# Performance work log

Measured on AMD Instinct MI355X. Metric: run time of the kernel, lower is better.

The kernel has to match this reference:

```python
import jax, jax.numpy as jnp
import numpy as np
from jax import lax

EPS = 1e-5

# sign binarization with straight-through-estimator gradient (identity),
# matching the .data-swap trick in BinarizeConv2d/BinarizeLinear.
@jax.custom_vjp
def ste_sign(x):
    return jnp.sign(x)

def _ste_fwd(x):
    return jnp.sign(x), None

def _ste_bwd(_, g):
    return (g,)

ste_sign.defvjp(_ste_fwd, _ste_bwd)


def conv3x3(x, w):
    # weight is binarized inside the layer; padding=1, stride=1, no bias
    return lax.conv_general_dilated(
        x, ste_sign(w), window_strides=(1, 1), padding=((1, 1), (1, 1)),
        dimension_numbers=('NCHW', 'OIHW', 'NCHW'))


def mp2(x):
    return lax.reduce_window(x, -jnp.inf, lax.max, (1, 1, 2, 2), (1, 1, 2, 2), 'VALID')


def bn2d(x, gamma, beta):
    # training-mode BatchNorm2d: batch statistics over (N, H, W)
    mu = jnp.mean(x, axis=(0, 2, 3), keepdims=True)
    var = jnp.var(x, axis=(0, 2, 3), keepdims=True)
    xn = (x - mu) * lax.rsqrt(var + EPS)
    return xn * gamma[None, :, None, None] + beta[None, :, None, None]


def bn1d(x, gamma=None, beta=None):
    mu = jnp.mean(x, axis=0, keepdims=True)
    var = jnp.var(x, axis=0, keepdims=True)
    xn = (x - mu) * lax.rsqrt(var + EPS)
    if gamma is None:
        return xn
    return xn * gamma[None, :] + beta[None, :]


def hardtanh(x):
    return jnp.clip(x, -1.0, 1.0)


def setup_inputs() -> dict:
    key = jax.random.key(0)
    ks = jax.random.split(key, 16)
    def w(k, shape):
        return jax.random.normal(k, shape, jnp.float32) * 0.1
    d = {'x': jax.random.normal(ks[0], (512, 3, 32, 32), jnp.float32)}
    convs = [(64, 3), (64, 64), (128, 64), (128, 128), (256, 128), (256, 256)]
    for i, (co, ci) in enumerate(convs):
        d[f'w{i+1}'] = w(ks[1 + i], (co, ci, 3, 3))
        d[f'g{i+1}'] = jnp.ones((co,), jnp.float32)
        d[f'b{i+1}'] = jnp.zeros((co,), jnp.float32)
    d['wf1'] = w(ks[7], (512, 256 * 4 * 4))
    d['gf1'] = jnp.ones((512,), jnp.float32)
    d['bf1'] = jnp.zeros((512,), jnp.float32)
    d['wf2'] = w(ks[8], (512, 512))
    d['gf2'] = jnp.ones((512,), jnp.float32)
    d['bf2'] = jnp.zeros((512,), jnp.float32)
    d['wf3'] = w(ks[9], (10, 512))
    return d


def reference(x, w1, g1, b1, w2, g2, b2, w3, g3, b3, w4, g4, b4,
              w5, g5, b5, w6, g6, b6, wf1, gf1, bf1, wf2, gf2, bf2, wf3):
    # block 1: first conv sees raw 3-channel input (not binarized)
    h = hardtanh(bn2d(conv3x3(x, w1), g1, b1))
    h = hardtanh(bn2d(mp2(conv3x3(ste_sign(h), w2)), g2, b2))
    # block 2
    h = hardtanh(bn2d(conv3x3(ste_sign(h), w3), g3, b3))
    h = hardtanh(bn2d(mp2(conv3x3(ste_sign(h), w4)), g4, b4))
    # block 3
    h = hardtanh(bn2d(conv3x3(ste_sign(h), w5), g5, b5))
    h = hardtanh(bn2d(mp2(conv3x3(ste_sign(h), w6)), g6, b6))
    # classifier (all linear inputs binarized: feature dim != 784)
    h = h.reshape(-1, 256 * 4 * 4)
    h = hardtanh(bn1d(ste_sign(h) @ ste_sign(wf1).T, gf1, bf1))
    h = hardtanh(bn1d(ste_sign(h) @ ste_sign(wf2).T, gf2, bf2))
    h = bn1d(ste_sign(h) @ ste_sign(wf3).T)  # affine=False
    return jax.nn.log_softmax(h, axis=-1)
```

## Files before the change

### kernel.cpp

```cpp
#include <hip/hip_runtime.h>
#include <stdint.h>
#include <math.h>


typedef unsigned long long u64;

__device__ __forceinline__ void flag_and_wave(u64* flag, u64 nz) {
    nz &= __shfl_xor(nz, 1);
    nz &= __shfl_xor(nz, 2);
    nz &= __shfl_xor(nz, 4);
    nz &= __shfl_xor(nz, 8);
    nz &= __shfl_xor(nz, 16);
    nz &= __shfl_xor(nz, 32);
    if ((threadIdx.x & 63) == 0) atomicAnd(flag, nz);
}

__global__ void kflag_init(u64* __restrict__ f) {
    int i = threadIdx.x;
    if (i < 16) f[i] = ~0ull;
}

__global__ __launch_bounds__(256) void k1_conv_allv(const float* __restrict__ x,
                                                    const float* __restrict__ wt,
                                                    float* __restrict__ out) {
    int gid = blockIdx.x * 256 + threadIdx.x;
    int n = gid >> 8, hw0 = (gid & 255) * 4;
    int y = hw0 >> 5, x0 = hw0 & 31;
    const float* ip = x + (size_t)n * 3 * 1024;
    for (int c0 = 0; c0 < 64; c0 += 16) {
        float4 a[16];
#pragma unroll
        for (int c = 0; c < 16; ++c) a[c] = make_float4(0.f, 0.f, 0.f, 0.f);
        for (int ky = 0; ky < 3; ++ky) {
            int yy = y + ky - 1;
            bool rowok = (unsigned)yy < 32u;
            float win[3][6];
#pragma unroll
            for (int ci = 0; ci < 3; ++ci)
#pragma unroll
                for (int j = 0; j < 6; ++j) {
                    int cc = x0 - 1 + j;
                    bool ok = rowok && ((unsigned)cc < 32u);
                    win[ci][j] = ok ? ip[ci * 1024 + yy * 32 + cc] : 0.f;
                }
#pragma unroll
            for (int kx = 0; kx < 3; ++kx)
#pragma unroll
                for (int ci = 0; ci < 3; ++ci) {
                    const float* wrow = wt + (ci * 9 + ky * 3 + kx) * 64 + c0;
                    float s0 = win[ci][kx], s1 = win[ci][kx + 1];
                    float s2 = win[ci][kx + 2], s3 = win[ci][kx + 3];
#pragma unroll
                    for (int c = 0; c < 16; ++c) {
                        float wv = wrow[c];
                        a[c].x = fmaf(wv, s0, a[c].x);
                        a[c].y = fmaf(wv, s1, a[c].y);
                        a[c].z = fmaf(wv, s2, a[c].z);
                        a[c].w = fmaf(wv, s3, a[c].w);
                    }
                }
        }
#pragma unroll
        for (int c = 0; c < 16; ++c)
            *(float4*)(out + ((size_t)n * 64 + c0 + c) * 1024 + hw0) = a[c];
    }
}

__global__ void k1_statsA(const float* __restrict__ v, double* __restrict__ Sp,
                          double* __restrict__ S2p, int N) {
    int c = blockIdx.x;
    int slot = blockIdx.y * 64 + threadIdx.x;
    double s = 0.0, s2 = 0.0;
    int K = N * 4;
    const float* vp = v + (size_t)c * 1024 + slot;
    int k0 = 0;
    for (; k0 + 32 <= K; k0 += 32) {
        const float* p0 = vp + (size_t)(k0 >> 2) * 65536;
        float buf[32];
#pragma unroll
        for (int j = 0; j < 32; ++j)
            buf[j] = p0[(size_t)(j >> 2) * 65536 + (j & 3) * 256];
#pragma unroll
        for (int j = 0; j < 32; ++j) {
            double t = (double)buf[j];
            s += t; s2 += t * t;
        }
    }
    for (; k0 < K; ++k0) {
        int m = slot + k0 * 256;
        double t = (double)v[((size_t)(m >> 10) * 64 + c) * 1024 + (m & 1023)];
        s += t; s2 += t * t;
    }
    Sp[c * 256 + slot] = s; S2p[c * 256 + slot] = s2;
}

__global__ void k1_statsB(const double* __restrict__ Sp, const double* __restrict__ S2p,
                          float* __restrict__ muF, float* __restrict__ rF, int N) {
    int c = blockIdx.x;
    __shared__ double sh[256], sh2[256];
    sh[threadIdx.x]  = Sp[c * 256 + threadIdx.x];
    sh2[threadIdx.x] = S2p[c * 256 + threadIdx.x];
    __syncthreads();
    for (int o = 128; o > 0; o >>= 1) {
        if ((int)threadIdx.x < o) { sh[threadIdx.x] += sh[threadIdx.x + o]; sh2[threadIdx.x] += sh2[threadIdx.x + o]; }
        __syncthreads();
    }
    if (threadIdx.x == 0) {
        int M = N * 1024;
        double mean = sh[0] / M;
        double var  = sh2[0] / M - mean * mean;
        if (var < 0.0) var = 0.0;
        muF[c] = (float)mean;
        rF[c]  = 1.0f / sqrtf((float)var + 1e-5f);
    }
}

__global__ void k1_signpack(const float* __restrict__ v, const float* __restrict__ muF,
                            const float* __restrict__ rF, const float* __restrict__ g,
                            const float* __restrict__ b, u64* __restrict__ B,
                            u64* __restrict__ NZ, u64* __restrict__ aflag) {
    int gid = blockIdx.x * 64 + threadIdx.x;
    int n = gid >> 8, hw0 = (gid & 255) * 4;
    const float* vp = v + ((size_t)n * 64) * 1024 + hw0;
    u64 bb0 = 0, bb1 = 0, bb2 = 0, bb3 = 0;
    u64 nz0 = 0, nz1 = 0, nz2 = 0, nz3 = 0;
    for (int c0 = 0; c0 < 64; c0 += 16) {
        float4 buf[16];
#pragma unroll
        for (int j = 0; j < 16; ++j)
            buf[j] = *(const float4*)(vp + (size_t)(c0 + j) * 1024);
#pragma unroll
        for (int j = 0; j < 16; ++j) {
            int c = c0 + j;
            float mc = muF[c], rc = rF[c], gc = g[c], bc = b[c];
            float d0 = buf[j].x - mc; float t0 = (d0 * rc) * gc + bc;
            float d1 = buf[j].y - mc; float t1 = (d1 * rc) * gc + bc;
            float d2 = buf[j].z - mc; float t2 = (d2 * rc) * gc + bc;
            float d3 = buf[j].w - mc; float t3 = (d3 * rc) * gc + bc;
            bb0 |= (u64)(t0 > 0.f) << c;  nz0 |= (u64)(t0 != 0.f) << c;
            bb1 |= (u64)(t1 > 0.f) << c;  nz1 |= (u64)(t1 != 0.f) << c;
            bb2 |= (u64)(t2 > 0.f) << c;  nz2 |= (u64)(t2 != 0.f) << c;
            bb3 |= (u64)(t3 > 0.f) << c;  nz3 |= (u64)(t3 != 0.f) << c;
        }
    }
    size_t o = (size_t)n * 1024 + hw0;
    B[o]     = bb0; B[o + 1]  = bb1; B[o + 2]  = bb2; B[o + 3]  = bb3;
    NZ[o]    = nz0; NZ[o + 1] = nz1; NZ[o + 2] = nz2; NZ[o + 3] = nz3;
    flag_and_wave(aflag, nz0 & nz1 & nz2 & nz3);
}

__global__ void k1_conv(const float* __restrict__ x, const float* __restrict__ w1,
                        float* __restrict__ out, int grp) {
    int hw = blockIdx.x * 64 + threadIdx.x;
    int cg = blockIdx.y;
    int n  = blockIdx.z;
    int co = grp * 8 + cg;
    int y = hw >> 5, x0 = hw & 31;
    const float* ip0 = x + ((size_t)n * 3 + 0) * 1024;
    const float* ip1 = x + ((size_t)n * 3 + 1) * 1024;
    const float* ip2 = x + ((size_t)n * 3 + 2) * 1024;
    const float* wp  = w1 + (size_t)co * 27;
    float acc = 0.f;
    for (int ky = 0; ky < 3; ++ky) {
        int yy = y + ky - 1;
        if (yy < 0 || yy > 31) continue;
        for (int kx = 0; kx < 3; ++kx) {
            int xc = x0 + kx - 1;
            if (xc < 0 || xc > 31) continue;
            int sp = yy * 32 + xc;
            int wk = ky * 3 + kx;
            float w0 = wp[wk], w1v = wp[9 + wk], w2 = wp[18 + wk];
            acc += (w0  > 0.f) ? ip0[sp] : ((w0  < 0.f) ? -ip0[sp] : 0.f);
            acc += (w1v > 0.f) ? ip1[sp] : ((w1v < 0.f) ? -ip1[sp] : 0.f);
            acc += (w2  > 0.f) ? ip2[sp] : ((w2  < 0.f) ? -ip2[sp] : 0.f);
        }
    }
    out[((size_t)n * 8 + cg) * 1024 + hw] = acc;
}

__device__ __forceinline__ float ld1(const float* v, int cg, int e) {
    return v[((size_t)(e >> 10) * 8 + cg) * 1024 + (e & 1023)];
}

__global__ void k1_stats(const float* __restrict__ v, float* __restrict__ muF,
                         float* __restrict__ rF, int grp, int N) {
    int cg = blockIdx.x;
    __shared__ double sh[256], sh2[256];
    double s = 0.0, s2 = 0.0;
    int M = N * 1024;
    for (int m = threadIdx.x; m < M; m += 256) {
        double t = (double)ld1(v, cg, m);
        s += t; s2 += t * t;
    }
    sh[threadIdx.x] = s; sh2[threadIdx.x] = s2;
    __syncthreads();
    for (int o = 128; o > 0; o >>= 1) {
        if ((int)threadIdx.x < o) { sh[threadIdx.x] += sh[threadIdx.x + o]; sh2[threadIdx.x] += sh2[threadIdx.x + o]; }
        __syncthreads();
    }
    if (threadIdx.x == 0) {
        double mean = sh[0] / M;
        double var  = sh2[0] / M - mean * mean;
        if (var < 0.0) var = 0.0;
        muF[grp * 8 + cg] = (float)mean;
        rF[grp * 8 + cg]  = 1.0f / sqrtf((float)var + 1e-5f);
    }
}

__global__ void k1_sign(const float* __restrict__ v, const float* __restrict__ muF,
                        const float* __restrict__ rF, const float* __restrict__ g,
                        const float* __restrict__ b, int8_t* __restrict__ sgn, int grp) {
    int hw = blockIdx.x * 256 + threadIdx.x;
    if (hw >= 1024) return;
    int cg = blockIdx.y, n = blockIdx.z;
    int c = grp * 8 + cg;
    float d  = v[((size_t)n * 8 + cg) * 1024 + hw] - muF[c];
    float t  = (d * rF[c]) * g[c] + b[c];
    sgn[((size_t)n * 64 + c) * 1024 + hw] = (int8_t)((t > 0.f) - (t < 0.f));
}

__global__ void kpack_sgn8(const int8_t* __restrict__ s, u64* __restrict__ B,
                           u64* __restrict__ NZ, int C, int HW, u64* __restrict__ aflag) {
    int hw = blockIdx.x * 64 + threadIdx.x;
    int wd = blockIdx.y, n = blockIdx.z;
    int WRD = C >> 6;
    u64 b = 0, nz = ~0ull;
    if (hw < HW) {
        nz = 0;
        const int8_t* sp = s + ((size_t)n * C + wd * 64) * HW + hw;
        for (int j = 0; j < 64; ++j) {
            int v = sp[(size_t)j * HW];
            b  |= (u64)(v > 0) << j;
            nz |= (u64)(v != 0) << j;
        }
        size_t o = ((size_t)n * HW + hw) * WRD + wd;
        B[o] = b; NZ[o] = nz;
    }
    flag_and_wave(aflag, nz);
}

__device__ __forceinline__ void pack_wconv_body(const float* __restrict__ w,
                                                u64* __restrict__ WB, u64* __restrict__ WNZ,
                                                int Ci, int Co, u64* flag, int idx) {
    int WRD = Ci >> 6;
    u64 b = 0, nz = ~0ull;
    if (idx < Co * 9 * WRD) {
        nz = 0;
        int wd = idx % WRD, t = (idx / WRD) % 9, co = idx / (9 * WRD);
        const float* wp = w + ((size_t)co * Ci + wd * 64) * 9 + t;
        float buf[64];
#pragma unroll
        for (int j = 0; j < 64; ++j) buf[j] = wp[(size_t)j * 9];
#pragma unroll
        for (int j = 0; j < 64; ++j) {
            b  |= (u64)(buf[j] > 0.f) << j;
            nz |= (u64)(buf[j] != 0.f) << j;
        }
        WB[idx] = b; WNZ[idx] = nz;
    }
    flag_and_wave(flag, nz);
}

__device__ __forceinline__ void pack_wlinT_body(const float* __restrict__ w,
                                                u64* __restrict__ WBt, u64* __restrict__ WZt,
                                                int K, int O, u64* flag, int idx) {
    int WRD = K >> 6;
    u64 b = 0, nz = ~0ull;
    if (idx < O * WRD) {
        nz = 0;
        int wd = idx % WRD, o = idx / WRD;
        const float* wp = w + (size_t)o * K + wd * 64;
#pragma unroll 8
        for (int j = 0; j < 64; ++j) {
            float v = wp[j];
            b  |= (u64)(v > 0.f) << j;
            nz |= (u64)(v != 0.f) << j;
        }
        WBt[(size_t)wd * O + o] = b; WZt[(size_t)wd * O + o] = nz;
    }
    flag_and_wave(flag, nz);
}

__global__ void kpack_all(const float* __restrict__ w1, const float* __restrict__ w2,
                          const float* __restrict__ w3, const float* __restrict__ w4,
                          const float* __restrict__ w5, const float* __restrict__ w6,
                          const float* __restrict__ wf1, const float* __restrict__ wf2,
                          const float* __restrict__ wf3, float* __restrict__ wt,
                          u64* wb2B, u64* wb2Z, u64* wb3B, u64* wb3Z,
                          u64* wb4B, u64* wb4Z, u64* wb5B, u64* wb5Z,
                          u64* wb6B, u64* wb6Z, u64* wf1B, u64* wf1Z,
                          u64* wf2B, u64* wf2Z, u64* wf3B, u64* wf3Z,
                          u64* flags) {
    int b = blockIdx.x, t = threadIdx.x;
    if      (b <   3) pack_wconv_body(w2, wb2B, wb2Z,  64,  64, &flags[0], b * 256 + t);
    else if (b <   8) pack_wconv_body(w3, wb3B, wb3Z,  64, 128, &flags[1], (b - 3) * 256 + t);
    else if (b <  17) pack_wconv_body(w4, wb4B, wb4Z, 128, 128, &flags[2], (b - 8) * 256 + t);
    else if (b <  35) pack_wconv_body(w5, wb5B, wb5Z, 128, 256, &flags[3], (b - 17) * 256 + t);
    else if (b <  71) pack_wconv_body(w6, wb6B, wb6Z, 256, 256, &flags[4], (b - 35) * 256 + t);
    else if (b < 199) pack_wlinT_body(wf1, wf1B, wf1Z, 4096, 512, &flags[5], (b - 71) * 256 + t);
    else if (b < 215) pack_wlinT_body(wf2, wf2B, wf2Z,  512, 512, &flags[6], (b - 199) * 256 + t);
    else if (b < 216) pack_wlinT_body(wf3, wf3B, wf3Z,  512,  10, &flags[7], (b - 215) * 256 + t);
    else {
        int i = (b - 216) * 256 + t;
        if (i < 64 * 27) {
            int co = i / 27, k = i % 27;
            float v = w1[i];
            wt[k * 64 + co] = (v > 0.f) ? 1.f : ((v < 0.f) ? -1.f : 0.f);
        }
    }
}

template <int WRD, int CB>
__device__ __forceinline__ void conv_slow(const u64* __restrict__ ib, const u64* __restrict__ iz,
                                          const u64* __restrict__ wbp, const u64* __restrict__ wzp,
                                          int H, int Wi, int y, int x, int* acc) {
#pragma unroll
    for (int c = 0; c < CB; ++c) acc[c] = 0;
    for (int ky = 0; ky < 3; ++ky) {
        int yy = y + ky - 1;
        if ((unsigned)yy >= (unsigned)H) continue;
        for (int kx = 0; kx < 3; ++kx) {
            int xc = x + kx - 1;
            if ((unsigned)xc >= (unsigned)Wi) continue;
            int p = yy * Wi + xc, t = ky * 3 + kx;
            u64 xb[WRD], xz[WRD];
#pragma unroll
            for (int w = 0; w < WRD; ++w) {
                xb[w] = ib[(size_t)p * WRD + w];
                xz[w] = iz[(size_t)p * WRD + w];
            }
#pragma unroll
            for (int c = 0; c < CB; ++c) {
#pragma unroll
                for (int w = 0; w < WRD; ++w) {
                    u64 e = xz[w] & wzp[(c * 9 + t) * WRD + w];
                    acc[c] += __popcll(e) - 2 * __popcll((xb[w] ^ wbp[(c * 9 + t) * WRD + w]) & e);
                }
            }
        }
    }
}

template <int WRD, int CB>
__device__ __forceinline__ void conv_fast(const u64* __restrict__ ib,
                                          const u64* __restrict__ wbp,
                                          int H, int Wi, int y, int x, int* acc) {
    int a2[CB];
#pragma unroll
    for (int c = 0; c < CB; ++c) a2[c] = 0;
    int T = 0;
    for (int ky = 0; ky < 3; ++ky) {
        int yy = y + ky - 1;
        if ((unsigned)yy >= (unsigned)H) continue;
        for (int kx = 0; kx < 3; ++kx) {
            int xc = x + kx - 1;
            if ((unsigned)xc >= (unsigned)Wi) continue;
            int p = yy * Wi + xc, t = ky * 3 + kx;
            ++T;
            u64 xb[WRD];
#pragma unroll
            for (int w = 0; w < WRD; ++w) xb[w] = ib[(size_t)p * WRD + w];
#pragma unroll
            for (int c = 0; c < CB; ++c)
#pragma unroll
                for (int w = 0; w < WRD; ++w)
                    a2[c] += __popcll(xb[w] ^ wbp[(c * 9 + t) * WRD + w]);
        }
    }
#pragma unroll
    for (int c = 0; c < CB; ++c) acc[c] = 64 * WRD * T - 2 * a2[c];
}

template <int WRD, int CB>
__global__ void kbconv2(const u64* __restrict__ B, const u64* __restrict__ NZ,
                        const u64* __restrict__ WB, const u64* __restrict__ WNZ,
                        int16_t* __restrict__ out, int Co, int H, int Wi,
                        const u64* __restrict__ wflag, const u64* __restrict__ aflag) {
    int hw = blockIdx.x * 64 + threadIdx.x;
    if (hw >= H * Wi) return;
    int co0 = blockIdx.y * CB, n = blockIdx.z;
    int y = hw / Wi, x = hw % Wi;
    const u64* ib = B  + (size_t)n * H * Wi * WRD;
    const u64* iz = NZ + (size_t)n * H * Wi * WRD;
    const u64* wbp = WB  + (size_t)co0 * 9 * WRD;
    const u64* wzp = WNZ + (size_t)co0 * 9 * WRD;
    bool fast = ((*wflag) & (*aflag)) == ~0ull;
    int acc[CB];
    if (fast) conv_fast<WRD, CB>(ib, wbp, H, Wi, y, x, acc);
    else      conv_slow<WRD, CB>(ib, iz, wbp, wzp, H, Wi, y, x, acc);
#pragma unroll
    for (int c = 0; c < CB; ++c)
        out[((size_t)n * Co + co0 + c) * H * Wi + hw] = (int16_t)acc[c];
}

template <int WRD, int CB>
__global__ void kbconv_pool2(const u64* __restrict__ B, const u64* __restrict__ NZ,
                             const u64* __restrict__ WB, const u64* __restrict__ WNZ,
                             int16_t* __restrict__ out, int Co, int H, int Wi,
                             const u64* __restrict__ wflag, const u64* __restrict__ aflag) {
    int Ho = H >> 1, Wo = Wi >> 1;
    int hw = blockIdx.x * 64 + threadIdx.x;
    if (hw >= Ho * Wo) return;
    int co0 = blockIdx.y * CB, n = blockIdx.z;
    int yo = hw / Wo, xo = hw % Wo;
    const u64* ib = B  + (size_t)n * H * Wi * WRD;
    const u64* iz = NZ + (size_t)n * H * Wi * WRD;
    const u64* wbp = WB  + (size_t)co0 * 9 * WRD;
    const u64* wzp = WNZ + (size_t)co0 * 9 * WRD;
    bool fast = ((*wflag) & (*aflag)) == ~0ull;
    int best[CB];
#pragma unroll
    for (int c = 0; c < CB; ++c) best[c] = -(1 << 30);
    if (fast) {
        for (int dy = 0; dy < 2; ++dy)
            for (int dx = 0; dx < 2; ++dx) {
                int acc[CB];
                conv_fast<WRD, CB>(ib, wbp, H, Wi, 2 * yo + dy, 2 * xo + dx, acc);
#pragma unroll
                for (int c = 0; c < CB; ++c) best[c] = acc[c] > best[c] ? acc[c] : best[c];
            }
    } else {
        for (int dy = 0; dy < 2; ++dy)
            for (int dx = 0; dx < 2; ++dx) {
                int acc[CB];
                conv_slow<WRD, CB>(ib, iz, wbp, wzp, H, Wi, 2 * yo + dy, 2 * xo + dx, acc);
#pragma unroll
                for (int c = 0; c < CB; ++c) best[c] = acc[c] > best[c] ? acc[c] : best[c];
            }
    }
#pragma unroll
    for (int c = 0; c < CB; ++c)
        out[((size_t)n * Co + co0 + c) * Ho * Wo + hw] = (int16_t)best[c];
}

template <int WRD, int CB>
__global__ void kbconv_pool2s(const u64* __restrict__ B, const u64* __restrict__ NZ,
                              const u64* __restrict__ WB, const u64* __restrict__ WNZ,
                              int16_t* __restrict__ out, int Co, int H, int Wi,
                              const u64* __restrict__ wflag, const u64* __restrict__ aflag) {
    int Ho = H >> 1, Wo = Wi >> 1;
    int t0 = threadIdx.x;
    int pix = t0 & 15, pos = t0 >> 4;
    int co0 = blockIdx.y * CB, n = blockIdx.z;
    int yo = pix / Wo, xo = pix % Wo;
    int y = 2 * yo + (pos >> 1), x = 2 * xo + (pos & 1);
    const u64* ib = B  + (size_t)n * H * Wi * WRD;
    const u64* iz = NZ + (size_t)n * H * Wi * WRD;
    const u64* wbp = WB  + (size_t)co0 * 9 * WRD;
    const u64* wzp = WNZ + (size_t)co0 * 9 * WRD;
    bool fast = ((*wflag) & (*aflag)) == ~0ull;
    int acc[CB];
    if (fast) conv_fast<WRD, CB>(ib, wbp, H, Wi, y, x, acc);
    else      conv_slow<WRD, CB>(ib, iz, wbp, wzp, H, Wi, y, x, acc);
#pragma unroll
    for (int c = 0; c < CB; ++c) {
        int v = acc[c];
        int v1 = __shfl_xor(v, 16); v = v1 > v ? v1 : v;
        int v2 = __shfl_xor(v, 32); v = v2 > v ? v2 : v;
        acc[c] = v;
    }
    if (pos == 0) {
#pragma unroll
        for (int c = 0; c < CB; ++c)
            out[((size_t)n * Co + co0 + c) * Ho * Wo + pix] = (int16_t)acc[c];
    }
}

__global__ void kaccum16(const int16_t* __restrict__ v, long long* __restrict__ Sp,
                         long long* __restrict__ S2p, int C, int HW, int M) {
    int c = blockIdx.x;
    long long s = 0, s2 = 0;
    int M8 = M >> 3;
    for (int g = blockIdx.y * 256 + threadIdx.x; g < M8; g += gridDim.y * 256) {
        int m0 = g * 8;
        const int16_t* p = v + ((size_t)(m0 / HW) * C + c) * HW + (m0 % HW);
        short4 a = *(const short4*)p;
        short4 b = *(const short4*)(p + 4);
        int v0 = a.x, v1 = a.y, v2 = a.z, v3 = a.w;
        int v4 = b.x, v5 = b.y, v6 = b.z, v7 = b.w;
        s  += v0 + v1 + v2 + v3 + v4 + v5 + v6 + v7;
        s2 += (long long)v0 * v0 + (long long)v1 * v1 + (long long)v2 * v2 + (long long)v3 * v3
            + (long long)v4 * v4 + (long long)v5 * v5 + (long long)v6 * v6 + (long long)v7 * v7;
    }
    __shared__ long long sh[256], sh2[256];
    sh[threadIdx.x] = s; sh2[threadIdx.x] = s2;
    __syncthreads();
    for (int o = 128; o > 0; o >>= 1) {
        if ((int)threadIdx.x < o) { sh[threadIdx.x] += sh[threadIdx.x + o]; sh2[threadIdx.x] += sh2[threadIdx.x + o]; }
        __syncthreads();
    }
    if (threadIdx.x == 0) {
        Sp[c * gridDim.y + blockIdx.y]  = sh[0];
        S2p[c * gridDim.y + blockIdx.y] = sh2[0];
    }
}

__global__ void kfinal2(const long long* __restrict__ Sp, const long long* __restrict__ S2p,
                        int NB, const float* __restrict__ g, const float* __restrict__ b,
                        double* __restrict__ mu, double* __restrict__ Ad,
                        double* __restrict__ Bd, int C, int M) {
    int c = blockIdx.x * 64 + threadIdx.x;
    if (c >= C) return;
    long long s = 0, s2 = 0;
    for (int i = 0; i < NB; ++i) { s += Sp[c * NB + i]; s2 += S2p[c * NB + i]; }
    double mean = (double)s / M;
    double var  = (double)s2 / M - mean * mean;
    if (var < 0.0) var = 0.0;
    mu[c] = mean;
    Ad[c] = (g ? (double)g[c] : 1.0) / sqrt(var + 1e-5);
    Bd[c] = b ? (double)b[c] : 0.0;
}

__global__ void ksp_conv(const int16_t* __restrict__ v, const double* __restrict__ mu,
                         const double* __restrict__ Ad, const double* __restrict__ Bd,
                         u64* __restrict__ B, u64* __restrict__ NZ, int C, int HW, int N,
                         u64* __restrict__ aflag) {
    int tid = blockIdx.x * 64 + threadIdx.x;
    int WRD = C >> 6;
    int HW4 = HW >> 2;
    int total = N * WRD * HW4;
    u64 nzall = ~0ull;
    if (tid < total) {
        int hw4 = tid % HW4;
        int wd  = (tid / HW4) % WRD;
        int n   = tid / (HW4 * WRD);
        const int16_t* vp = v + ((size_t)n * C + wd * 64) * HW + hw4 * 4;
        u64 b0 = 0, b1 = 0, b2 = 0, b3 = 0;
        u64 n0 = 0, n1 = 0, n2 = 0, n3 = 0;
        for (int j0 = 0; j0 < 64; j0 += 16) {
            short4 buf[16];
#pragma unroll
            for (int j = 0; j < 16; ++j)
                buf[j] = *(const short4*)(vp + (size_t)(j0 + j) * HW);
#pragma unroll
            for (int j = 0; j < 16; ++j) {
                int c = wd * 64 + j0 + j;
                double Mu = mu[c], A = Ad[c], Bb = Bd[c];
                double t0 = ((double)buf[j].x - Mu) * A + Bb;
                double t1 = ((double)buf[j].y - Mu) * A + Bb;
                double t2 = ((double)buf[j].z - Mu) * A + Bb;
                double t3 = ((double)buf[j].w - Mu) * A + Bb;
                int sh = j0 + j;
                b0 |= (u64)(t0 > 0.0) << sh;  n0 |= (u64)(t0 != 0.0) << sh;
                b1 |= (u64)(t1 > 0.0) << sh;  n1 |= (u64)(t1 != 0.0) << sh;
                b2 |= (u64)(t2 > 0.0) << sh;  n2 |= (u64)(t2 != 0.0) << sh;
                b3 |= (u64)(t3 > 0.0) << sh;  n3 |= (u64)(t3 != 0.0) << sh;
            }
        }
        size_t o = ((size_t)n * HW + hw4 * 4) * WRD + wd;
        B[o] = b0;  B[o + WRD] = b1;  B[o + 2 * WRD] = b2;  B[o + 3 * WRD] = b3;
        NZ[o] = n0; NZ[o + WRD] = n1; NZ[o + 2 * WRD] = n2; NZ[o + 3 * WRD] = n3;
        nzall = n0 & n1 & n2 & n3;
    }
    flag_and_wave(aflag, nzall);
}

__global__ void ksp_flat(const int16_t* __restrict__ v, const double* __restrict__ mu,
                         const double* __restrict__ Ad, const double* __restrict__ Bd,
                         u64* __restrict__ B, u64* __restrict__ NZ, u64* __restrict__ aflag) {
    int wd = threadIdx.x;
    int n  = blockIdx.x;
    const int16_t* vp = v + (size_t)n * 4096 + wd * 64;
    int16_t buf[64];
#pragma unroll
    for (int j = 0; j < 64; ++j) buf[j] = vp[j];
    u64 b = 0, nz = 0;
#pragma unroll
    for (int j = 0; j < 64; ++j) {
        int k = wd * 64 + j;
        int c = k >> 4;
        double t = ((double)buf[j] - mu[c]) * Ad[c] + Bd[c];
        b  |= (u64)(t > 0.0) << j;
        nz |= (u64)(t != 0.0) << j;
    }
    B[(size_t)n * 64 + wd] = b; NZ[(size_t)n * 64 + wd] = nz;
    flag_and_wave(aflag, nz);
}

__global__ void ksp_fc(const int* __restrict__ v, const double* __restrict__ mu,
                       const double* __restrict__ Ad, const double* __restrict__ Bd,
                       u64* __restrict__ B, u64* __restrict__ NZ, int C, int WRD, int N,
                       u64* __restrict__ aflag) {
    int tid = blockIdx.x * 64 + threadIdx.x;
    u64 nz = ~0ull;
    if (tid < N * WRD) {
        int n = tid / WRD, wd = tid % WRD;
        const int* vp = v + (size_t)n * C + wd * 64;
        int buf[64];
#pragma unroll
        for (int j = 0; j < 64; ++j) buf[j] = vp[j];
        u64 b = 0; nz = 0;
#pragma unroll
        for (int j = 0; j < 64; ++j) {
            int c = wd * 64 + j;
            double t = ((double)buf[j] - mu[c]) * Ad[c] + Bd[c];
            b  |= (u64)(t > 0.0) << j;
            nz |= (u64)(t != 0.0) << j;
        }
        B[(size_t)n * WRD + wd] = b; NZ[(size_t)n * WRD + wd] = nz;
    }
    flag_and_wave(aflag, nz);
}

__global__ void kbfc(const u64* __restrict__ aB, const u64* __restrict__ aNZ,
                     const u64* __restrict__ wBt, const u64* __restrict__ wZt,
                     int* __restrict__ out, int WRD, int O,
                     const u64* __restrict__ wflag, const u64* __restrict__ aflag) {
    int o = blockIdx.x * 64 + threadIdx.x;
    if (o >= O) return;
    int n = blockIdx.y;
    const u64* ab = aB  + (size_t)n * WRD;
    const u64* az = aNZ + (size_t)n * WRD;
    bool fast = ((*wflag) & (*aflag)) == ~0ull;
    int acc;
    if (fast) {
        int a2 = 0;
        for (int w = 0; w < WRD; w += 8) {
            u64 aw[8], ww[8];
#pragma unroll
            for (int j = 0; j < 8; ++j) {
                aw[j] = ab[w + j];
                ww[j] = wBt[(size_t)(w + j) * O + o];
            }
#pragma unroll
            for (int j = 0; j < 8; ++j) a2 += __popcll(aw[j] ^ ww[j]);
        }
        acc = 64 * WRD - 2 * a2;
    } else {
        acc = 0;
        for (int w = 0; w < WRD; ++w) {
            u64 wb = wBt[(size_t)w * O + o];
            u64 wz = wZt[(size_t)w * O + o];
            u64 e = az[w] & wz;
            acc += __popcll(e) - 2 * __popcll((ab[w] ^ wb) & e);
        }
    }
    out[(size_t)n * O + o] = acc;
}

__global__ void k3_stats(const int* __restrict__ v, int N, int C,
                         const float* __restrict__ g, const float* __restrict__ b,
                         double* __restrict__ mu, double* __restrict__ Ad,
                         double* __restrict__ Bd) {
    int c = blockIdx.x;
    __shared__ double sh[256], sh2[256];
    double s = 0.0, s2 = 0.0;
    for (int n = threadIdx.x; n < N; n += 256) {
        double t = (double)v[(size_t)n * C + c];
        s += t; s2 += t * t;
    }
    sh[threadIdx.x] = s; sh2[threadIdx.x] = s2;
    __syncthreads();
    for (int o = 128; o > 0; o >>= 1) {
        if ((int)threadIdx.x < o) { sh[threadIdx.x] += sh[threadIdx.x + o]; sh2[threadIdx.x] += sh2[threadIdx.x + o]; }
        __syncthreads();
    }
    if (threadIdx.x == 0) {
        double mean = sh[0] / N;
        double var  = sh2[0] / N - mean * mean;
        if (var < 0.0) var = 0.0;
        mu[c] = mean;
        Ad[c] = (g ? (double)g[c] : 1.0) / sqrt(var + 1e-5);
        Bd[c] = b ? (double)b[c] : 0.0;
    }
}

__global__ void k4_out(const int* __restrict__ v, const double* __restrict__ mu,
                       const double* __restrict__ Ad, float* __restrict__ out, int N) {
    int n = blockIdx.x * 256 + threadIdx.x;
    if (n >= N) return;
    double z[10];
    double mx = -1e300;
    for (int o = 0; o < 10; ++o) {
        z[o] = ((double)v[n * 10 + o] - mu[o]) * Ad[o];
        if (z[o] > mx) mx = z[o];
    }
    double s = 0.0;
    for (int o = 0; o < 10; ++o) s += exp(z[o] - mx);
    double l = mx + log(s);
    for (int o = 0; o < 10; ++o) out[n * 10 + o] = (float)(z[o] - l);
}

extern "C" void kernel_launch(void* const* d_in, const int* in_sizes, int n_in,
                              void* d_out, int out_size, void* d_ws, size_t ws_size,
                              hipStream_t stream) {
    const int N = in_sizes[0] / (3 * 32 * 32);

    const float* x   = (const float*)d_in[0];
    const float* w1  = (const float*)d_in[1];
    const float* g1  = (const float*)d_in[2];
    const float* b1  = (const float*)d_in[3];
    const float* w2  = (const float*)d_in[4];
    const float* g2  = (const float*)d_in[5];
    const float* b2  = (const float*)d_in[6];
    const float* w3  = (const float*)d_in[7];
    const float* g3  = (const float*)d_in[8];
    const float* b3  = (const float*)d_in[9];
    const float* w4  = (const float*)d_in[10];
    const float* g4  = (const float*)d_in[11];
    const float* b4  = (const float*)d_in[12];
    const float* w5  = (const float*)d_in[13];
    const float* g5  = (const float*)d_in[14];
    const float* b5  = (const float*)d_in[15];
    const float* w6  = (const float*)d_in[16];
    const float* g6  = (const float*)d_in[17];
    const float* b6  = (const float*)d_in[18];
    const float* wf1 = (const float*)d_in[19];
    const float* gf1 = (const float*)d_in[20];
    const float* bf1 = (const float*)d_in[21];
    const float* wf2 = (const float*)d_in[22];
    const float* gf2 = (const float*)d_in[23];
    const float* bf2 = (const float*)d_in[24];
    const float* wf3 = (const float*)d_in[25];

    char* ws = (char*)d_ws;
    size_t off = 0;
    auto alloc = [&](size_t bytes) -> char* {
        char* p = ws + off;
        off = (off + bytes + 511) & ~(size_t)511;
        return p;
    };

    int16_t* t2  = (int16_t*)alloc((size_t)N * 64 * 256 * 2);
    u64* p2B = (u64*)alloc((size_t)N * 256 * 8);
    u64* p2Z = (u64*)alloc((size_t)N * 256 * 8);
    int16_t* t3  = (int16_t*)alloc((size_t)N * 128 * 256 * 2);
    u64* p3B = (u64*)alloc((size_t)N * 256 * 2 * 8);
    u64* p3Z = (u64*)alloc((size_t)N * 256 * 2 * 8);
    int16_t* t4  = (int16_t*)alloc((size_t)N * 128 * 64 * 2);
    u64* p4B = (u64*)alloc((size_t)N * 64 * 2 * 8);
    u64* p4Z = (u64*)alloc((size_t)N * 64 * 2 * 8);
    int16_t* t5  = (int16_t*)alloc((size_t)N * 256 * 64 * 2);
    u64* p5B = (u64*)alloc((size_t)N * 64 * 4 * 8);
    u64* p5Z = (u64*)alloc((size_t)N * 64 * 4 * 8);
    int16_t* t6  = (int16_t*)alloc((size_t)N * 256 * 16 * 2);
    u64* p6B = (u64*)alloc((size_t)N * 64 * 8);
    u64* p6Z = (u64*)alloc((size_t)N * 64 * 8);
    int* fc1 = (int*)alloc((size_t)N * 512 * 4);
    int* fc2 = (int*)alloc((size_t)N * 512 * 4);
    int* fc3 = (int*)alloc((size_t)N * 10 * 4);
    u64* pF1B = (u64*)alloc((size_t)N * 8 * 8);
    u64* pF1Z = (u64*)alloc((size_t)N * 8 * 8);
    u64* pF2B = (u64*)alloc((size_t)N * 8 * 8);
    u64* pF2Z = (u64*)alloc((size_t)N * 8 * 8);
    size_t down_end = off;

    size_t head_big = (size_t)N * 64 * 1024 * 4;
    bool big = ws_size >= head_big + ((size_t)20 << 20);
    float*  c1buf = (float*)ws;
    float*  c1buf8 = (float*)ws;
    int8_t* sgnA  = (int8_t*)(ws + (size_t)N * 8 * 1024 * 4);

    off = big ? (head_big > down_end ? head_big : down_end) : down_end;
    off = (off + 511) & ~(size_t)511;
    u64* p1B = (u64*)alloc((size_t)N * 1024 * 8);
    u64* p1Z = (u64*)alloc((size_t)N * 1024 * 8);
    u64* wb2B = (u64*)alloc(64  * 9 * 1 * 8);  u64* wb2Z = (u64*)alloc(64  * 9 * 1 * 8);
    u64* wb3B = (u64*)alloc(128 * 9 * 1 * 8);  u64* wb3Z = (u64*)alloc(128 * 9 * 1 * 8);
    u64* wb4B = (u64*)alloc(128 * 9 * 2 * 8);  u64* wb4Z = (u64*)alloc(128 * 9 * 2 * 8);
    u64* wb5B = (u64*)alloc(256 * 9 * 2 * 8);  u64* wb5Z = (u64*)alloc(256 * 9 * 2 * 8);
    u64* wb6B = (u64*)alloc(256 * 9 * 4 * 8);  u64* wb6Z = (u64*)alloc(256 * 9 * 4 * 8);
    u64* wf1B = (u64*)alloc(512 * 64 * 8);     u64* wf1Z = (u64*)alloc(512 * 64 * 8);
    u64* wf2B = (u64*)alloc(512 * 8 * 8);      u64* wf2Z = (u64*)alloc(512 * 8 * 8);
    u64* wf3B = (u64*)alloc(10 * 8 * 8);       u64* wf3Z = (u64*)alloc(10 * 8 * 8);
    float* wt = (float*)alloc(27 * 64 * 4);
    double* Sp  = (double*)alloc(64 * 256 * 8);
    double* S2p = (double*)alloc(64 * 256 * 8);
    long long* SpI  = (long long*)alloc(256 * 32 * 8);
    long long* S2pI = (long long*)alloc(256 * 32 * 8);
    u64* flags = (u64*)alloc(16 * 8);
    double* mu = (double*)alloc(512 * 8);
    double* Ad = (double*)alloc(512 * 8);
    double* Bd = (double*)alloc(512 * 8);
    float*  muF = (float*)alloc(64 * 4);
    float*  rF  = (float*)alloc(64 * 4);

    auto cdiv = [](int a, int b) { return (a + b - 1) / b; };

    kflag_init<<<1, 64, 0, stream>>>(flags);
    kpack_all<<<223, 256, 0, stream>>>(w1, w2, w3, w4, w5, w6, wf1, wf2, wf3, wt,
                                       wb2B, wb2Z, wb3B, wb3Z, wb4B, wb4Z,
                                       wb5B, wb5Z, wb6B, wb6Z, wf1B, wf1Z,
                                       wf2B, wf2Z, wf3B, wf3Z, flags);

    if (big) {
        k1_conv_allv<<<(N * 256) / 256, 256, 0, stream>>>(x, wt, c1buf);
        k1_statsA<<<dim3(64, 4), 64, 0, stream>>>(c1buf, Sp, S2p, N);
        k1_statsB<<<64, 256, 0, stream>>>(Sp, S2p, muF, rF, N);
        k1_signpack<<<(N * 256) / 64, 64, 0, stream>>>(c1buf, muF, rF, g1, b1, p1B, p1Z, &flags[8]);
    } else {
        for (int grp = 0; grp < 8; ++grp) {
            k1_conv<<<dim3(16, 8, N), 64, 0, stream>>>(x, w1, c1buf8, grp);
            k1_stats<<<8, 256, 0, stream>>>(c1buf8, muF, rF, grp, N);
            k1_sign<<<dim3(4, 8, N), 256, 0, stream>>>(c1buf8, muF, rF, g1, b1, sgnA, grp);
        }
        kpack_sgn8<<<dim3(16, 1, N), 64, 0, stream>>>(sgnA, p1B, p1Z, 64, 1024, &flags[8]);
    }

    kbconv_pool2<1, 8><<<dim3(4, 8, N), 64, 0, stream>>>(p1B, p1Z, wb2B, wb2Z, t2, 64, 32, 32, &flags[0], &flags[8]);
    kaccum16<<<dim3(64, 32), 256, 0, stream>>>(t2, SpI, S2pI, 64, 256, N * 256);
    kfinal2<<<1, 64, 0, stream>>>(SpI, S2pI, 32, g2, b2, mu, Ad, Bd, 64, N * 256);
    ksp_conv<<<cdiv(N * 1 * 64, 64), 64, 0, stream>>>(t2, mu, Ad, Bd, p2B, p2Z, 64, 256, N, &flags[9]);

    kbconv2<1, 8><<<dim3(4, 16, N), 64, 0, stream>>>(p2B, p2Z, wb3B, wb3Z, t3, 128, 16, 16, &flags[1], &flags[9]);
    kaccum16<<<dim3(128, 16), 256, 0, stream>>>(t3, SpI, S2pI, 128, 256, N * 256);
    kfinal2<<<2, 64, 0, stream>>>(SpI, S2pI, 16, g3, b3, mu, Ad, Bd, 128, N * 256);
    ksp_conv<<<cdiv(N * 2 * 64, 64), 64, 0, stream>>>(t3, mu, Ad, Bd, p3B, p3Z, 128, 256, N, &flags[10]);

    kbconv_pool2<2, 8><<<dim3(1, 16, N), 64, 0, stream>>>(p3B, p3Z, wb4B, wb4Z, t4, 128, 16, 16, &flags[2], &flags[10]);
    kaccum16<<<dim3(128, 16), 256, 0, stream>>>(t4, SpI, S2pI, 128, 64, N * 64);
    kfinal2<<<2, 64, 0, stream>>>(SpI, S2pI, 16, g4, b4, mu, Ad, Bd, 128, N * 64);
    ksp_conv<<<cdiv(N * 2 * 16, 64), 64, 0, stream>>>(t4, mu, Ad, Bd, p4B, p4Z, 128, 64, N, &flags[11]);

    kbconv2<2, 8><<<dim3(1, 32, N), 64, 0, stream>>>(p4B, p4Z, wb5B, wb5Z, t5, 256, 8, 8, &flags[3], &flags[11]);
    kaccum16<<<dim3(256, 8), 256, 0, stream>>>(t5, SpI, S2pI, 256, 64, N * 64);
    kfinal2<<<4, 64, 0, stream>>>(SpI, S2pI, 8, g5, b5, mu, Ad, Bd, 256, N * 64);
    ksp_conv<<<cdiv(N * 4 * 16, 64), 64, 0, stream>>>(t5, mu, Ad, Bd, p5B, p5Z, 256, 64, N, &flags[12]);

    kbconv_pool2s<4, 8><<<dim3(1, 32, N), 64, 0, stream>>>(p5B, p5Z, wb6B, wb6Z, t6, 256, 8, 8, &flags[4], &flags[12]);
    kaccum16<<<dim3(256, 2), 256, 0, stream>>>(t6, SpI, S2pI, 256, 16, N * 16);
    kfinal2<<<4, 64, 0, stream>>>(SpI, S2pI, 2, g6, b6, mu, Ad, Bd, 256, N * 16);
    ksp_flat<<<N, 64, 0, stream>>>(t6, mu, Ad, Bd, p6B, p6Z, &flags[13]);

    kbfc<<<dim3(8, N), 64, 0, stream>>>(p6B, p6Z, wf1B, wf1Z, fc1, 64, 512, &flags[5], &flags[13]);
    k3_stats<<<512, 256, 0, stream>>>(fc1, N, 512, gf1, bf1, mu, Ad, Bd);
    ksp_fc<<<cdiv(N * 8, 64), 64, 0, stream>>>(fc1, mu, Ad, Bd, pF1B, pF1Z, 512, 8, N, &flags[14]);

    kbfc<<<dim3(8, N), 64, 0, stream>>>(pF1B, pF1Z, wf2B, wf2Z, fc2, 8, 512, &flags[6], &flags[14]);
    k3_stats<<<512, 256, 0, stream>>>(fc2, N, 512, gf2, bf2, mu, Ad, Bd);
    ksp_fc<<<cdiv(N * 8, 64), 64, 0, stream>>>(fc2, mu, Ad, Bd, pF2B, pF2Z, 512, 8, N, &flags[15]);

    kbfc<<<dim3(1, N), 64, 0, stream>>>(pF2B, pF2Z, wf3B, wf3Z, fc3, 8, 10, &flags[7], &flags[15]);
    k3_stats<<<10, 256, 0, stream>>>(fc3, N, 10, nullptr, nullptr, mu, Ad, Bd);
    k4_out<<<cdiv(N, 256), 256, 0, stream>>>(fc3, mu, Ad, (float*)d_out, N);
}
```

Before: 652.7 us.

## Reuse loaded activation windows across neighbouring outputs in binary convs

Adds a conv kernel where each thread computes two horizontally adjacent output pixels from one 3x4 register window. Each weight word is loaded once and applied to both pixels, and the result is stored as a packed 32-bit write. The pool2 fast path now loads a 4x4 input window once and reuses it for all four pooled positions instead of calling conv_fast four times. This cuts redundant global loads of activations and weights, at the cost of more registers and fewer threads for layer 3.

```diff
diff --git a/kernel.cpp b/kernel.cpp
--- a/kernel.cpp
+++ b/kernel.cpp
@@ -394,6 +394,76 @@
 }
 
 template <int WRD, int CB>
+__global__ void kbconv2p(const u64* __restrict__ B, const u64* __restrict__ NZ,
+                         const u64* __restrict__ WB, const u64* __restrict__ WNZ,
+                         int16_t* __restrict__ out, int Co, int H, int Wi,
+                         const u64* __restrict__ wflag, const u64* __restrict__ aflag) {
+    int W2 = Wi >> 1;
+    int hp = blockIdx.x * 64 + threadIdx.x;
+    if (hp >= H * W2) return;
+    int co0 = blockIdx.y * CB, n = blockIdx.z;
+    int y = hp / W2, x0 = (hp % W2) * 2;
+    const u64* ib = B  + (size_t)n * H * Wi * WRD;
+    const u64* iz = NZ + (size_t)n * H * Wi * WRD;
+    const u64* wbp = WB  + (size_t)co0 * 9 * WRD;
+    const u64* wzp = WNZ + (size_t)co0 * 9 * WRD;
+    bool fast = ((*wflag) & (*aflag)) == ~0ull;
+    int acc0[CB], acc1[CB];
+    if (fast) {
+        u64 xr[3][4][WRD]; bool vr[3][4];
+#pragma unroll
+        for (int dy = 0; dy < 3; ++dy) {
+            int yy = y - 1 + dy;
+            bool rok = (unsigned)yy < (unsigned)H;
+#pragma unroll
+            for (int dx = 0; dx < 4; ++dx) {
+                int xc = x0 - 1 + dx;
+                bool ok = rok && ((unsigned)xc < (unsigned)Wi);
+                vr[dy][dx] = ok;
+#pragma unroll
+                for (int w = 0; w < WRD; ++w)
+                    xr[dy][dx][w] = ok ? ib[(size_t)(yy * Wi + xc) * WRD + w] : 0ull;
+            }
+        }
+        int a20[CB], a21[CB];
+#pragma unroll
+        for (int c = 0; c < CB; ++c) { a20[c] = 0; a21[c] = 0; }
+        int T0 = 0, T1 = 0;
+#pragma unroll
+        for (int ky = 0; ky < 3; ++ky)
+#pragma unroll
+            for (int kx = 0; kx < 3; ++kx) {
+                int t = ky * 3 + kx;
+                bool v0 = vr[ky][kx], v1 = vr[ky][kx + 1];
+                if (v0) ++T0;
+                if (v1) ++T1;
+#pragma unroll
+                for (int c = 0; c < CB; ++c)
+#pragma unroll
+                    for (int w = 0; w < WRD; ++w) {
+                        u64 wv = wbp[(c * 9 + t) * WRD + w];
+                        if (v0) a20[c] += __popcll(xr[ky][kx][w] ^ wv);
+                        if (v1) a21[c] += __popcll(xr[ky][kx + 1][w] ^ wv);
+                    }
+            }
+#pragma unroll
+        for (int c = 0; c < CB; ++c) {
+            acc0[c] = 64 * WRD * T0 - 2 * a20[c];
+            acc1[c] = 64 * WRD * T1 - 2 * a21[c];
+        }
+    } else {
+        conv_slow<WRD, CB>(ib, iz, wbp, wzp, H, Wi, y, x0, acc0);
+        conv_slow<WRD, CB>(ib, iz, wbp, wzp, H, Wi, y, x0 + 1, acc1);
+    }
+#pragma unroll
+    for (int c = 0; c < CB; ++c) {
+        unsigned pack = (unsigned)(uint16_t)(int16_t)acc0[c]
+                      | ((unsigned)(uint16_t)(int16_t)acc1[c] << 16);
+        *(unsigned*)&out[((size_t)n * Co + co0 + c) * H * Wi + y * Wi + x0] = pack;
+    }
+}
+
+template <int WRD, int CB>
 __global__ void kbconv_pool2(const u64* __restrict__ B, const u64* __restrict__ NZ,
                              const u64* __restrict__ WB, const u64* __restrict__ WNZ,
                              int16_t* __restrict__ out, int Co, int H, int Wi,
@@ -412,12 +482,47 @@
 #pragma unroll
     for (int c = 0; c < CB; ++c) best[c] = -(1 << 30);
     if (fast) {
-        for (int dy = 0; dy < 2; ++dy)
-            for (int dx = 0; dx < 2; ++dx) {
-                int acc[CB];
-                conv_fast<WRD, CB>(ib, wbp, H, Wi, 2 * yo + dy, 2 * xo + dx, acc);
-#pragma unroll
-                for (int c = 0; c < CB; ++c) best[c] = acc[c] > best[c] ? acc[c] : best[c];
+        u64 xr[4][4][WRD]; bool vr[4][4];
+#pragma unroll
+        for (int dy = 0; dy < 4; ++dy) {
+            int yy = 2 * yo - 1 + dy;
+            bool rok = (unsigned)yy < (unsigned)H;
+#pragma unroll
+            for (int dx = 0; dx < 4; ++dx) {
+                int xc = 2 * xo - 1 + dx;
+                bool ok = rok && ((unsigned)xc < (unsigned)Wi);
+                vr[dy][dx] = ok;
+#pragma unroll
+                for (int w = 0; w < WRD; ++w)
+                    xr[dy][dx][w] = ok ? ib[(size_t)(yy * Wi + xc) * WRD + w] : 0ull;
+            }
+        }
+#pragma unroll
+        for (int dy2 = 0; dy2 < 2; ++dy2)
+#pragma unroll
+            for (int dx2 = 0; dx2 < 2; ++dx2) {
+                int a2[CB];
+#pragma unroll
+                for (int c = 0; c < CB; ++c) a2[c] = 0;
+                int T = 0;
+#pragma unroll
+                for (int ky = 0; ky < 3; ++ky)
+#pragma unroll
+                    for (int kx = 0; kx < 3; ++kx) {
+                        if (!vr[dy2 + ky][dx2 + kx]) continue;
+                        ++T;
+                        int t = ky * 3 + kx;
+#pragma unroll
+                        for (int c = 0; c < CB; ++c)
+#pragma unroll
+                            for (int w = 0; w < WRD; ++w)
+                                a2[c] += __popcll(xr[dy2 + ky][dx2 + kx][w] ^ wbp[(c * 9 + t) * WRD + w]);
+                    }
+#pragma unroll
+                for (int c = 0; c < CB; ++c) {
+                    int acc = 64 * WRD * T - 2 * a2[c];
+                    best[c] = acc > best[c] ? acc : best[c];
+                }
             }
     } else {
         for (int dy = 0; dy < 2; ++dy)
@@ -802,7 +907,7 @@
     kfinal2<<<1, 64, 0, stream>>>(SpI, S2pI, 32, g2, b2, mu, Ad, Bd, 64, N * 256);
     ksp_conv<<<cdiv(N * 1 * 64, 64), 64, 0, stream>>>(t2, mu, Ad, Bd, p2B, p2Z, 64, 256, N, &flags[9]);
 
-    kbconv2<1, 8><<<dim3(4, 16, N), 64, 0, stream>>>(p2B, p2Z, wb3B, wb3Z, t3, 128, 16, 16, &flags[1], &flags[9]);
+    kbconv2p<1, 8><<<dim3(2, 16, N), 64, 0, stream>>>(p2B, p2Z, wb3B, wb3Z, t3, 128, 16, 16, &flags[1], &flags[9]);
     kaccum16<<<dim3(128, 16), 256, 0, stream>>>(t3, SpI, S2pI, 128, 256, N * 256);
     kfinal2<<<2, 64, 0, stream>>>(SpI, S2pI, 16, g3, b3, mu, Ad, Bd, 128, N * 256);
     ksp_conv<<<cdiv(N * 2 * 64, 64), 64, 0, stream>>>(t3, mu, Ad, Bd, p3B, p3Z, 128, 256, N, &flags[10]);
```

Result: slower. 666.6 us (+2.1%).
